# Optimization experiments

Hardware: AMD Instinct MI355X
Metric: run time of the kernel (lower is better)

## Reference

```python
import jax, jax.numpy as jnp
import numpy as np

NUM_USERS = 150000
NUM_ITEMS = 140000
NUM_BRANDS = 10000
N_NODES = NUM_USERS + NUM_ITEMS + NUM_BRANDS
EMBED_DIM = 64
N_LAYERS = 3
N_EDGES = 1200000


def setup_inputs() -> dict:
    key = jax.random.key(0)
    k1, k2, k3, k4, k5, k6 = jax.random.split(key, 6)
    # Xavier-uniform-ish init scale for embeddings
    s = float(np.sqrt(6.0 / (N_NODES + EMBED_DIM)))
    user_emb = jax.random.normal(k1, (NUM_USERS, EMBED_DIM), dtype=jnp.float32) * s
    item_emb = jax.random.normal(k2, (NUM_ITEMS, EMBED_DIM), dtype=jnp.float32) * s
    brand_emb = jax.random.normal(k3, (NUM_BRANDS, EMBED_DIM), dtype=jnp.float32) * s
    edge_src = jax.random.randint(k4, (N_EDGES,), 0, N_NODES, dtype=jnp.int32)
    edge_dst = jax.random.randint(k5, (N_EDGES,), 0, N_NODES, dtype=jnp.int32)
    # symmetric-normalized-adjacency-like positive values
    edge_vals = jax.random.uniform(k6, (N_EDGES,), dtype=jnp.float32)
    return {
        "user_emb": user_emb,
        "item_emb": item_emb,
        "brand_emb": brand_emb,
        "edge_vals": edge_vals,
        "edge_src": edge_src,
        "edge_dst": edge_dst,
    }


def _spmm(edge_src, edge_dst, edge_vals, x):
    # out[d] = sum_{e: dst[e]=d} vals[e] * x[src[e]]  (COO SpMM)
    msgs = x[edge_src] * edge_vals[:, None]  # [E, D]
    return jax.ops.segment_sum(msgs, edge_dst, num_segments=N_NODES)


def reference(user_emb, item_emb, brand_emb, edge_vals, edge_src, edge_dst):
    ego = jnp.concatenate([user_emb, item_emb, brand_emb], axis=0)  # [N, D]
    acc = ego
    h = ego
    for _ in range(N_LAYERS):
        h = _spmm(edge_src, edge_dst, edge_vals, h)
        acc = acc + h
    final = acc / jnp.float32(N_LAYERS + 1)  # mean over layer stack
    final_user = final[:NUM_USERS]
    final_item = final[NUM_USERS:NUM_USERS + NUM_ITEMS]
    return (final_user, final_item)
```

## Files before the change

kernel.cpp:

```cpp
#include <hip/hip_runtime.h>

#define NUM_USERS  150000
#define NUM_ITEMS  140000
#define NUM_BRANDS 10000
#define N_NODES    300000
#define DIM        64
#define N_EDGES    1200000
#define OUT_ROWS   290000

#define CHUNK      1024
#define NB         ((N_NODES + CHUNK - 1) / CHUNK)

#define NBIN       8
#define BINSZ      (N_EDGES / NBIN)

__device__ __forceinline__ float bf_lo(unsigned u) { return __uint_as_float(u << 16); }
__device__ __forceinline__ float bf_hi(unsigned u) { return __uint_as_float(u & 0xffff0000u); }
__device__ __forceinline__ unsigned pack_bf(float a, float b) {
    unsigned ua = __float_as_uint(a); ua += 0x7fffu + ((ua >> 16) & 1u);
    unsigned ub = __float_as_uint(b); ub += 0x7fffu + ((ub >> 16) & 1u);
    return (ua >> 16) | (ub & 0xffff0000u);
}

__global__ void lgcn_hist(const int* __restrict__ dst,
                          int* __restrict__ counts,
                          int* __restrict__ rank) {
    int e = blockIdx.x * blockDim.x + threadIdx.x;
    if (e >= N_EDGES) return;
    rank[e] = atomicAdd(&counts[dst[e]], 1);
}

__global__ void lgcn_scan_p1(const int* __restrict__ counts,
                             int* __restrict__ rowptr,
                             int* __restrict__ blockSums) {
    __shared__ int ts[256];
    int b    = blockIdx.x;
    int base = b * CHUNK;
    int t    = threadIdx.x;
    int c[4];
    int s = 0;
#pragma unroll
    for (int i = 0; i < 4; ++i) {
        int g = base + t * 4 + i;
        c[i] = (g < N_NODES) ? counts[g] : 0;
        s += c[i];
    }
    ts[t] = s;
    __syncthreads();
    for (int off = 1; off < 256; off <<= 1) {
        int v = (t >= off) ? ts[t - off] : 0;
        __syncthreads();
        ts[t] += v;
        __syncthreads();
    }
    int run = ts[t] - s;
#pragma unroll
    for (int i = 0; i < 4; ++i) {
        int g = base + t * 4 + i;
        if (g < N_NODES) rowptr[g] = run;
        run += c[i];
    }
    if (t == 255) blockSums[b] = ts[255];
}

__global__ void lgcn_scan_p2(int* __restrict__ blockSums) {
    __shared__ int sh[512];
    int t = threadIdx.x;
    int v = (t < NB) ? blockSums[t] : 0;
    sh[t] = v;
    __syncthreads();
    for (int off = 1; off < 512; off <<= 1) {
        int u = (t >= off) ? sh[t - off] : 0;
        __syncthreads();
        sh[t] += u;
        __syncthreads();
    }
    if (t < NB) blockSums[t] = sh[t] - v;
}

__global__ void lgcn_scan_p3(int* __restrict__ rowptr,
                             const int* __restrict__ blockSums) {
    int b    = blockIdx.x;
    int base = b * CHUNK;
    int t    = threadIdx.x;
    int off  = blockSums[b];
#pragma unroll
    for (int i = 0; i < 4; ++i) {
        int g = base + t * 4 + i;
        if (g < N_NODES) rowptr[g] += off;
    }
    if (b == 0 && t == 0) rowptr[N_NODES] = N_EDGES;
}

__global__ void lgcn_egobf(const float* __restrict__ user,
                           const float* __restrict__ item,
                           const float* __restrict__ brand,
                           uint4* __restrict__ ego_bf) {
    int g = blockIdx.x * blockDim.x + threadIdx.x;
    if (g >= N_NODES * 8) return;
    int row = g >> 3;
    int q   = g & 7;
    const float* srcp;
    if (row < NUM_USERS)                    srcp = user  + ((size_t)row << 6);
    else if (row < NUM_USERS + NUM_ITEMS)   srcp = item  + ((size_t)(row - NUM_USERS) << 6);
    else                                    srcp = brand + ((size_t)(row - NUM_USERS - NUM_ITEMS) << 6);
    float4 e0 = *(reinterpret_cast<const float4*>(srcp) + 2 * q);
    float4 e1 = *(reinterpret_cast<const float4*>(srcp) + 2 * q + 1);
    uint4 w;
    w.x = pack_bf(e0.x, e0.y);
    w.y = pack_bf(e0.z, e0.w);
    w.z = pack_bf(e1.x, e1.y);
    w.w = pack_bf(e1.z, e1.w);
    ego_bf[g] = w;
}

__global__ void lgcn_csr_bin(const int*   __restrict__ src,
                             const int*   __restrict__ dst,
                             const float* __restrict__ vals,
                             const int*   __restrict__ rank,
                             const int*   __restrict__ rowptr,
                             uint2*       __restrict__ csr) {
    int b    = blockIdx.x;
    int bin  = b & (NBIN - 1);
    int e    = (b >> 3) * blockDim.x + threadIdx.x;
    if (e >= N_EDGES) return;
    int pos = rowptr[dst[e]] + rank[e];
    int lo  = bin * BINSZ;
    if (pos >= lo && pos < lo + BINSZ) {
        csr[pos] = make_uint2((unsigned)src[e], __float_as_uint(vals[e]));
    }
}

__device__ __forceinline__ const float4* ego_row(const float* __restrict__ user,
                                                 const float* __restrict__ item,
                                                 const float* __restrict__ brand,
                                                 int r) {
    if (r < NUM_USERS)
        return reinterpret_cast<const float4*>(user) + (r << 4);
    else if (r < NUM_USERS + NUM_ITEMS)
        return reinterpret_cast<const float4*>(item) + ((r - NUM_USERS) << 4);
    else
        return reinterpret_cast<const float4*>(brand) + ((r - NUM_USERS - NUM_ITEMS) << 4);
}

template <int LAYER>
__global__ void lgcn_gather(const int*   __restrict__ rowptr,
                            const uint2* __restrict__ csr,
                            const uint4* __restrict__ h_src,
                            const float* __restrict__ user,
                            const float* __restrict__ item,
                            const float* __restrict__ brand,
                            const uint4* __restrict__ h1,
                            const uint4* __restrict__ h2,
                            uint4*       __restrict__ h_out,
                            float*       __restrict__ out) {
    int g    = blockIdx.x * blockDim.x + threadIdx.x;
    int node = g >> 3;
    int q    = g & 7;
    int beg = rowptr[node];
    int end = rowptr[node + 1];
    float4 s0 = make_float4(0.f, 0.f, 0.f, 0.f);
    float4 s1 = make_float4(0.f, 0.f, 0.f, 0.f);
    if (beg < end) {
        int last = end - 1;
        uint2 rec0 = csr[beg];
        uint2 rec1 = csr[beg + 1 < end ? beg + 1 : last];
        uint2 rec2 = csr[beg + 2 < end ? beg + 2 : last];
        uint2 rec3 = csr[beg + 3 < end ? beg + 3 : last];
        uint4 w0 = h_src[((int)rec0.x << 3) + q];
        uint4 w1 = h_src[((int)rec1.x << 3) + q];
        uint4 w2 = h_src[((int)rec2.x << 3) + q];
        for (int j = beg; j < end; ++j) {
            int jn = j + 4 < end ? j + 4 : last;
            uint2 rec4 = csr[jn];
            uint4 w3 = h_src[((int)rec3.x << 3) + q];
            float v = __uint_as_float(rec0.y);
            s0.x = fmaf(bf_lo(w0.x), v, s0.x);
            s0.y = fmaf(bf_hi(w0.x), v, s0.y);
            s0.z = fmaf(bf_lo(w0.y), v, s0.z);
            s0.w = fmaf(bf_hi(w0.y), v, s0.w);
            s1.x = fmaf(bf_lo(w0.z), v, s1.x);
            s1.y = fmaf(bf_hi(w0.z), v, s1.y);
            s1.z = fmaf(bf_lo(w0.w), v, s1.z);
            s1.w = fmaf(bf_hi(w0.w), v, s1.w);
            rec0 = rec1; rec1 = rec2; rec2 = rec3; rec3 = rec4;
            w0 = w1; w1 = w2; w2 = w3;
        }
    }
    if (LAYER != 3) {
        uint4 w;
        w.x = pack_bf(s0.x, s0.y);
        w.y = pack_bf(s0.z, s0.w);
        w.z = pack_bf(s1.x, s1.y);
        w.w = pack_bf(s1.z, s1.w);
        h_out[g] = w;
    } else if (node < OUT_ROWS) {
        const float4* er = ego_row(user, item, brand, node);
        float4 e0 = er[2 * q];
        float4 e1 = er[2 * q + 1];
        uint4 w1 = h1[g];
        uint4 w2 = h2[g];
        float4 o0, o1;
        o0.x = (e0.x + bf_lo(w1.x) + bf_lo(w2.x) + s0.x) * 0.25f;
        o0.y = (e0.y + bf_hi(w1.x) + bf_hi(w2.x) + s0.y) * 0.25f;
        o0.z = (e0.z + bf_lo(w1.y) + bf_lo(w2.y) + s0.z) * 0.25f;
        o0.w = (e0.w + bf_hi(w1.y) + bf_hi(w2.y) + s0.w) * 0.25f;
        o1.x = (e1.x + bf_lo(w1.z) + bf_lo(w2.z) + s1.x) * 0.25f;
        o1.y = (e1.y + bf_hi(w1.z) + bf_hi(w2.z) + s1.y) * 0.25f;
        o1.z = (e1.z + bf_lo(w1.w) + bf_lo(w2.w) + s1.z) * 0.25f;
        o1.w = (e1.w + bf_hi(w1.w) + bf_hi(w2.w) + s1.w) * 0.25f;
        float4* o = reinterpret_cast<float4*>(out) + g * 2;
        o[0] = o0;
        o[1] = o1;
    }
}

extern "C" void kernel_launch(void* const* d_in, const int* in_sizes, int n_in,
                              void* d_out, int out_size, void* d_ws, size_t ws_size,
                              hipStream_t stream) {
    const float* user  = (const float*)d_in[0];
    const float* item  = (const float*)d_in[1];
    const float* brand = (const float*)d_in[2];
    const float* vals  = (const float*)d_in[3];
    const int*   src   = (const int*)d_in[4];
    const int*   dst   = (const int*)d_in[5];
    float* out = (float*)d_out;

    size_t W = 0;
    uint4* ego_bf = (uint4*)d_ws;              W += (size_t)N_NODES * 32;
    uint4* h1  = (uint4*)((int*)d_ws + W);     W += (size_t)N_NODES * 32;
    uint4* h2  = (uint4*)((int*)d_ws + W);     W += (size_t)N_NODES * 32;
    uint2* csr = (uint2*)((int*)d_ws + W);     W += (size_t)N_EDGES * 2;
    int* rank      = (int*)d_ws + W;           W += N_EDGES;
    int* rowptr    = (int*)d_ws + W;           W += N_NODES + 2;
    int* counts    = (int*)d_ws + W;           W += N_NODES;
    int* blockSums = (int*)d_ws + W;           W += 512;
    (void)ws_size; (void)n_in; (void)in_sizes; (void)out_size;

    const int edgeBlocks   = (N_EDGES + 255) / 256;
    const int gatherBlocks = (N_NODES * 8) / 256;

    hipMemsetAsync(counts, 0, (size_t)N_NODES * sizeof(int), stream);

    lgcn_egobf  <<<gatherBlocks, 256, 0, stream>>>(user, item, brand, ego_bf);

    lgcn_hist   <<<edgeBlocks, 256, 0, stream>>>(dst, counts, rank);
    lgcn_scan_p1<<<NB, 256, 0, stream>>>(counts, rowptr, blockSums);
    lgcn_scan_p2<<<1, 512, 0, stream>>>(blockSums);
    lgcn_scan_p3<<<NB, 256, 0, stream>>>(rowptr, blockSums);
    lgcn_csr_bin<<<NBIN * edgeBlocks, 256, 0, stream>>>(src, dst, vals, rank,
                                                        rowptr, csr);

    lgcn_gather<1><<<gatherBlocks, 256, 0, stream>>>(rowptr, csr, ego_bf, user, item,
                                                     brand, h1, h2, h1, out);
    lgcn_gather<2><<<gatherBlocks, 256, 0, stream>>>(rowptr, csr, h1, user, item,
                                                     brand, h1, h2, h2, out);
    lgcn_gather<3><<<gatherBlocks, 256, 0, stream>>>(rowptr, csr, h2, user, item,
                                                     brand, h1, h2, nullptr, out);
}
```

Before: 273.7 us.

## Drop bf16 ego conversion, precompute CSR positions, unroll gather by two

```diff
diff --git a/kernel.cpp b/kernel.cpp
--- a/kernel.cpp
+++ b/kernel.cpp
@@ -92,42 +92,27 @@
     if (b == 0 && t == 0) rowptr[N_NODES] = N_EDGES;
 }
 
-__global__ void lgcn_egobf(const float* __restrict__ user,
-                           const float* __restrict__ item,
-                           const float* __restrict__ brand,
-                           uint4* __restrict__ ego_bf) {
-    int g = blockIdx.x * blockDim.x + threadIdx.x;
-    if (g >= N_NODES * 8) return;
-    int row = g >> 3;
-    int q   = g & 7;
-    const float* srcp;
-    if (row < NUM_USERS)                    srcp = user  + ((size_t)row << 6);
-    else if (row < NUM_USERS + NUM_ITEMS)   srcp = item  + ((size_t)(row - NUM_USERS) << 6);
-    else                                    srcp = brand + ((size_t)(row - NUM_USERS - NUM_ITEMS) << 6);
-    float4 e0 = *(reinterpret_cast<const float4*>(srcp) + 2 * q);
-    float4 e1 = *(reinterpret_cast<const float4*>(srcp) + 2 * q + 1);
-    uint4 w;
-    w.x = pack_bf(e0.x, e0.y);
-    w.y = pack_bf(e0.z, e0.w);
-    w.z = pack_bf(e1.x, e1.y);
-    w.w = pack_bf(e1.z, e1.w);
-    ego_bf[g] = w;
+__global__ void lgcn_pos(const int* __restrict__ dst,
+                         const int* __restrict__ rank,
+                         const int* __restrict__ rowptr,
+                         int* __restrict__ pos) {
+    int e = blockIdx.x * blockDim.x + threadIdx.x;
+    if (e >= N_EDGES) return;
+    pos[e] = rowptr[dst[e]] + rank[e];
 }
 
 __global__ void lgcn_csr_bin(const int*   __restrict__ src,
-                             const int*   __restrict__ dst,
                              const float* __restrict__ vals,
-                             const int*   __restrict__ rank,
-                             const int*   __restrict__ rowptr,
+                             const int*   __restrict__ pos,
                              uint2*       __restrict__ csr) {
     int b    = blockIdx.x;
     int bin  = b & (NBIN - 1);
     int e    = (b >> 3) * blockDim.x + threadIdx.x;
     if (e >= N_EDGES) return;
-    int pos = rowptr[dst[e]] + rank[e];
-    int lo  = bin * BINSZ;
-    if (pos >= lo && pos < lo + BINSZ) {
-        csr[pos] = make_uint2((unsigned)src[e], __float_as_uint(vals[e]));
+    int p  = pos[e];
+    int lo = bin * BINSZ;
+    if (p >= lo && p < lo + BINSZ) {
+        csr[p] = make_uint2((unsigned)src[e], __float_as_uint(vals[e]));
     }
 }
 
@@ -142,6 +127,53 @@
     else
         return reinterpret_cast<const float4*>(brand) + ((r - NUM_USERS - NUM_ITEMS) << 4);
 }
+
+template <int LAYER>
+struct RowStore {
+    typedef uint4 type;
+    static __device__ __forceinline__ type load(const uint4* __restrict__ h,
+                                                const float*, const float*, const float*,
+                                                int r, int q) {
+        return h[(r << 3) + q];
+    }
+    static __device__ __forceinline__ void fma(float4& s0, float4& s1, type w, float v) {
+        s0.x = fmaf(bf_lo(w.x), v, s0.x);
+        s0.y = fmaf(bf_hi(w.x), v, s0.y);
+        s0.z = fmaf(bf_lo(w.y), v, s0.z);
+        s0.w = fmaf(bf_hi(w.y), v, s0.w);
+        s1.x = fmaf(bf_lo(w.z), v, s1.x);
+        s1.y = fmaf(bf_hi(w.z), v, s1.y);
+        s1.z = fmaf(bf_lo(w.w), v, s1.z);
+        s1.w = fmaf(bf_hi(w.w), v, s1.w);
+    }
+};
+
+struct Row8 { float4 a, b; };
+template <>
+struct RowStore<1> {
+    typedef Row8 type;
+    static __device__ __forceinline__ type load(const uint4*,
+                                                const float* __restrict__ u,
+                                                const float* __restrict__ i,
+                                                const float* __restrict__ b,
+                                                int r, int q) {
+        const float4* er = ego_row(u, i, b, r);
+        Row8 t;
+        t.a = er[2 * q];
+        t.b = er[2 * q + 1];
+        return t;
+    }
+    static __device__ __forceinline__ void fma(float4& s0, float4& s1, type w, float v) {
+        s0.x = fmaf(w.a.x, v, s0.x);
+        s0.y = fmaf(w.a.y, v, s0.y);
+        s0.z = fmaf(w.a.z, v, s0.z);
+        s0.w = fmaf(w.a.w, v, s0.w);
+        s1.x = fmaf(w.b.x, v, s1.x);
+        s1.y = fmaf(w.b.y, v, s1.y);
+        s1.z = fmaf(w.b.z, v, s1.z);
+        s1.w = fmaf(w.b.w, v, s1.w);
+    }
+};
 
 template <int LAYER>
 __global__ void lgcn_gather(const int*   __restrict__ rowptr,
@@ -154,6 +186,7 @@
                             const uint4* __restrict__ h2,
                             uint4*       __restrict__ h_out,
                             float*       __restrict__ out) {
+    typedef typename RowStore<LAYER>::type RowT;
     int g    = blockIdx.x * blockDim.x + threadIdx.x;
     int node = g >> 3;
     int q    = g & 7;
@@ -161,31 +194,30 @@
     int end = rowptr[node + 1];
     float4 s0 = make_float4(0.f, 0.f, 0.f, 0.f);
     float4 s1 = make_float4(0.f, 0.f, 0.f, 0.f);
+    float4 t0 = make_float4(0.f, 0.f, 0.f, 0.f);
+    float4 t1 = make_float4(0.f, 0.f, 0.f, 0.f);
     if (beg < end) {
         int last = end - 1;
-        uint2 rec0 = csr[beg];
-        uint2 rec1 = csr[beg + 1 < end ? beg + 1 : last];
-        uint2 rec2 = csr[beg + 2 < end ? beg + 2 : last];
-        uint2 rec3 = csr[beg + 3 < end ? beg + 3 : last];
-        uint4 w0 = h_src[((int)rec0.x << 3) + q];
-        uint4 w1 = h_src[((int)rec1.x << 3) + q];
-        uint4 w2 = h_src[((int)rec2.x << 3) + q];
-        for (int j = beg; j < end; ++j) {
-            int jn = j + 4 < end ? j + 4 : last;
-            uint2 rec4 = csr[jn];
-            uint4 w3 = h_src[((int)rec3.x << 3) + q];
-            float v = __uint_as_float(rec0.y);
-            s0.x = fmaf(bf_lo(w0.x), v, s0.x);
-            s0.y = fmaf(bf_hi(w0.x), v, s0.y);
-            s0.z = fmaf(bf_lo(w0.y), v, s0.z);
-            s0.w = fmaf(bf_hi(w0.y), v, s0.w);
-            s1.x = fmaf(bf_lo(w0.z), v, s1.x);
-            s1.y = fmaf(bf_hi(w0.z), v, s1.y);
-            s1.z = fmaf(bf_lo(w0.w), v, s1.z);
-            s1.w = fmaf(bf_hi(w0.w), v, s1.w);
-            rec0 = rec1; rec1 = rec2; rec2 = rec3; rec3 = rec4;
-            w0 = w1; w1 = w2; w2 = w3;
+        uint2 r0 = csr[beg];
+        uint2 r1 = csr[beg + 1 < end ? beg + 1 : last];
+        uint2 r2 = csr[beg + 2 < end ? beg + 2 : last];
+        uint2 r3 = csr[beg + 3 < end ? beg + 3 : last];
+        RowT wA = RowStore<LAYER>::load(h_src, user, item, brand, (int)r0.x, q);
+        RowT wB = RowStore<LAYER>::load(h_src, user, item, brand, (int)r1.x, q);
+        for (int j = beg; j < end; j += 2) {
+            uint2 r4 = csr[j + 4 < end ? j + 4 : last];
+            uint2 r5 = csr[j + 5 < end ? j + 5 : last];
+            RowT wC = RowStore<LAYER>::load(h_src, user, item, brand, (int)r2.x, q);
+            RowT wD = RowStore<LAYER>::load(h_src, user, item, brand, (int)r3.x, q);
+            float vA = __uint_as_float(r0.y);
+            float vB = (j + 1 < end) ? __uint_as_float(r1.y) : 0.f;
+            RowStore<LAYER>::fma(s0, s1, wA, vA);
+            RowStore<LAYER>::fma(t0, t1, wB, vB);
+            r0 = r2; r1 = r3; r2 = r4; r3 = r5;
+            wA = wC; wB = wD;
         }
+        s0.x += t0.x; s0.y += t0.y; s0.z += t0.z; s0.w += t0.w;
+        s1.x += t1.x; s1.y += t1.y; s1.z += t1.z; s1.w += t1.w;
     }
     if (LAYER != 3) {
         uint4 w;
@@ -227,11 +259,11 @@
     float* out = (float*)d_out;
 
     size_t W = 0;
-    uint4* ego_bf = (uint4*)d_ws;              W += (size_t)N_NODES * 32;
-    uint4* h1  = (uint4*)((int*)d_ws + W);     W += (size_t)N_NODES * 32;
+    uint4* h1  = (uint4*)d_ws;                 W += (size_t)N_NODES * 32;
     uint4* h2  = (uint4*)((int*)d_ws + W);     W += (size_t)N_NODES * 32;
     uint2* csr = (uint2*)((int*)d_ws + W);     W += (size_t)N_EDGES * 2;
     int* rank      = (int*)d_ws + W;           W += N_EDGES;
+    int* pos       = (int*)d_ws + W;           W += N_EDGES;
     int* rowptr    = (int*)d_ws + W;           W += N_NODES + 2;
     int* counts    = (int*)d_ws + W;           W += N_NODES;
     int* blockSums = (int*)d_ws + W;           W += 512;
@@ -242,16 +274,14 @@
 
     hipMemsetAsync(counts, 0, (size_t)N_NODES * sizeof(int), stream);
 
-    lgcn_egobf  <<<gatherBlocks, 256, 0, stream>>>(user, item, brand, ego_bf);
-
     lgcn_hist   <<<edgeBlocks, 256, 0, stream>>>(dst, counts, rank);
     lgcn_scan_p1<<<NB, 256, 0, stream>>>(counts, rowptr, blockSums);
     lgcn_scan_p2<<<1, 512, 0, stream>>>(blockSums);
     lgcn_scan_p3<<<NB, 256, 0, stream>>>(rowptr, blockSums);
-    lgcn_csr_bin<<<NBIN * edgeBlocks, 256, 0, stream>>>(src, dst, vals, rank,
-                                                        rowptr, csr);
-
-    lgcn_gather<1><<<gatherBlocks, 256, 0, stream>>>(rowptr, csr, ego_bf, user, item,
+    lgcn_pos    <<<edgeBlocks, 256, 0, stream>>>(dst, rank, rowptr, pos);
+    lgcn_csr_bin<<<NBIN * edgeBlocks, 256, 0, stream>>>(src, vals, pos, csr);
+
+    lgcn_gather<1><<<gatherBlocks, 256, 0, stream>>>(rowptr, csr, nullptr, user, item,
                                                      brand, h1, h2, h1, out);
     lgcn_gather<2><<<gatherBlocks, 256, 0, stream>>>(rowptr, csr, h1, user, item,
                                                      brand, h1, h2, h2, out);
```

Measured after the change: 241.0 us. -12.0%, faster.

## Drop bf16 ego conversion, gather fp32 ego directly, precompute CSR positions

Applied to the files above, without the earlier changes.

```diff
diff --git a/kernel.cpp b/kernel.cpp
--- a/kernel.cpp
+++ b/kernel.cpp
@@ -92,42 +92,27 @@
     if (b == 0 && t == 0) rowptr[N_NODES] = N_EDGES;
 }
 
-__global__ void lgcn_egobf(const float* __restrict__ user,
-                           const float* __restrict__ item,
-                           const float* __restrict__ brand,
-                           uint4* __restrict__ ego_bf) {
-    int g = blockIdx.x * blockDim.x + threadIdx.x;
-    if (g >= N_NODES * 8) return;
-    int row = g >> 3;
-    int q   = g & 7;
-    const float* srcp;
-    if (row < NUM_USERS)                    srcp = user  + ((size_t)row << 6);
-    else if (row < NUM_USERS + NUM_ITEMS)   srcp = item  + ((size_t)(row - NUM_USERS) << 6);
-    else                                    srcp = brand + ((size_t)(row - NUM_USERS - NUM_ITEMS) << 6);
-    float4 e0 = *(reinterpret_cast<const float4*>(srcp) + 2 * q);
-    float4 e1 = *(reinterpret_cast<const float4*>(srcp) + 2 * q + 1);
-    uint4 w;
-    w.x = pack_bf(e0.x, e0.y);
-    w.y = pack_bf(e0.z, e0.w);
-    w.z = pack_bf(e1.x, e1.y);
-    w.w = pack_bf(e1.z, e1.w);
-    ego_bf[g] = w;
+__global__ void lgcn_pos(const int* __restrict__ dst,
+                         const int* __restrict__ rank,
+                         const int* __restrict__ rowptr,
+                         int* __restrict__ pos) {
+    int e = blockIdx.x * blockDim.x + threadIdx.x;
+    if (e >= N_EDGES) return;
+    pos[e] = rowptr[dst[e]] + rank[e];
 }
 
 __global__ void lgcn_csr_bin(const int*   __restrict__ src,
-                             const int*   __restrict__ dst,
                              const float* __restrict__ vals,
-                             const int*   __restrict__ rank,
-                             const int*   __restrict__ rowptr,
+                             const int*   __restrict__ pos,
                              uint2*       __restrict__ csr) {
     int b    = blockIdx.x;
     int bin  = b & (NBIN - 1);
     int e    = (b >> 3) * blockDim.x + threadIdx.x;
     if (e >= N_EDGES) return;
-    int pos = rowptr[dst[e]] + rank[e];
-    int lo  = bin * BINSZ;
-    if (pos >= lo && pos < lo + BINSZ) {
-        csr[pos] = make_uint2((unsigned)src[e], __float_as_uint(vals[e]));
+    int p  = pos[e];
+    int lo = bin * BINSZ;
+    if (p >= lo && p < lo + BINSZ) {
+        csr[p] = make_uint2((unsigned)src[e], __float_as_uint(vals[e]));
     }
 }
 
@@ -143,17 +128,13 @@
         return reinterpret_cast<const float4*>(brand) + ((r - NUM_USERS - NUM_ITEMS) << 4);
 }
 
-template <int LAYER>
-__global__ void lgcn_gather(const int*   __restrict__ rowptr,
-                            const uint2* __restrict__ csr,
-                            const uint4* __restrict__ h_src,
-                            const float* __restrict__ user,
-                            const float* __restrict__ item,
-                            const float* __restrict__ brand,
-                            const uint4* __restrict__ h1,
-                            const uint4* __restrict__ h2,
-                            uint4*       __restrict__ h_out,
-                            float*       __restrict__ out) {
+__global__ void __launch_bounds__(256, 8)
+lgcn_gather1(const int*   __restrict__ rowptr,
+             const uint2* __restrict__ csr,
+             const float* __restrict__ user,
+             const float* __restrict__ item,
+             const float* __restrict__ brand,
+             uint4*       __restrict__ h_out) {
     int g    = blockIdx.x * blockDim.x + threadIdx.x;
     int node = g >> 3;
     int q    = g & 7;
@@ -162,44 +143,111 @@
     float4 s0 = make_float4(0.f, 0.f, 0.f, 0.f);
     float4 s1 = make_float4(0.f, 0.f, 0.f, 0.f);
     if (beg < end) {
-        int last = end - 1;
         uint2 rec0 = csr[beg];
-        uint2 rec1 = csr[beg + 1 < end ? beg + 1 : last];
-        uint2 rec2 = csr[beg + 2 < end ? beg + 2 : last];
-        uint2 rec3 = csr[beg + 3 < end ? beg + 3 : last];
-        uint4 w0 = h_src[((int)rec0.x << 3) + q];
-        uint4 w1 = h_src[((int)rec1.x << 3) + q];
-        uint4 w2 = h_src[((int)rec2.x << 3) + q];
+        uint2 rec1 = csr[(beg + 1 < end) ? beg + 1 : beg];
+        const float4* p0 = ego_row(user, item, brand, (int)rec0.x);
+        float4 a0 = p0[2 * q];
+        float4 b0 = p0[2 * q + 1];
         for (int j = beg; j < end; ++j) {
-            int jn = j + 4 < end ? j + 4 : last;
-            uint2 rec4 = csr[jn];
-            uint4 w3 = h_src[((int)rec3.x << 3) + q];
+            int jn = j + 2 < end ? j + 2 : end - 1;
+            uint2 rec2 = csr[jn];
+            const float4* p1 = ego_row(user, item, brand, (int)rec1.x);
+            float4 a1 = p1[2 * q];
+            float4 b1 = p1[2 * q + 1];
             float v = __uint_as_float(rec0.y);
-            s0.x = fmaf(bf_lo(w0.x), v, s0.x);
-            s0.y = fmaf(bf_hi(w0.x), v, s0.y);
-            s0.z = fmaf(bf_lo(w0.y), v, s0.z);
-            s0.w = fmaf(bf_hi(w0.y), v, s0.w);
-            s1.x = fmaf(bf_lo(w0.z), v, s1.x);
-            s1.y = fmaf(bf_hi(w0.z), v, s1.y);
-            s1.z = fmaf(bf_lo(w0.w), v, s1.z);
-            s1.w = fmaf(bf_hi(w0.w), v, s1.w);
-            rec0 = rec1; rec1 = rec2; rec2 = rec3; rec3 = rec4;
-            w0 = w1; w1 = w2; w2 = w3;
+            s0.x = fmaf(a0.x, v, s0.x);
+            s0.y = fmaf(a0.y, v, s0.y);
+            s0.z = fmaf(a0.z, v, s0.z);
+            s0.w = fmaf(a0.w, v, s0.w);
+            s1.x = fmaf(b0.x, v, s1.x);
+            s1.y = fmaf(b0.y, v, s1.y);
+            s1.z = fmaf(b0.z, v, s1.z);
+            s1.w = fmaf(b0.w, v, s1.w);
+            rec0 = rec1; rec1 = rec2; a0 = a1; b0 = b1;
         }
     }
-    if (LAYER != 3) {
-        uint4 w;
-        w.x = pack_bf(s0.x, s0.y);
-        w.y = pack_bf(s0.z, s0.w);
-        w.z = pack_bf(s1.x, s1.y);
-        w.w = pack_bf(s1.z, s1.w);
-        h_out[g] = w;
-    } else if (node < OUT_ROWS) {
+    uint4 w;
+    w.x = pack_bf(s0.x, s0.y);
+    w.y = pack_bf(s0.z, s0.w);
+    w.z = pack_bf(s1.x, s1.y);
+    w.w = pack_bf(s1.z, s1.w);
+    h_out[g] = w;
+}
+
+__device__ __forceinline__ void gather_bf_core(int beg, int end, int q,
+                                               const uint2* __restrict__ csr,
+                                               const uint4* __restrict__ h_src,
+                                               float4& s0, float4& s1) {
+    int last = end - 1;
+    uint2 rec0 = csr[beg];
+    uint2 rec1 = csr[beg + 1 < end ? beg + 1 : last];
+    uint2 rec2 = csr[beg + 2 < end ? beg + 2 : last];
+    uint2 rec3 = csr[beg + 3 < end ? beg + 3 : last];
+    uint4 w0 = h_src[((int)rec0.x << 3) + q];
+    uint4 w1 = h_src[((int)rec1.x << 3) + q];
+    uint4 w2 = h_src[((int)rec2.x << 3) + q];
+    for (int j = beg; j < end; ++j) {
+        int jn = j + 4 < end ? j + 4 : last;
+        uint2 rec4 = csr[jn];
+        uint4 w3 = h_src[((int)rec3.x << 3) + q];
+        float v = __uint_as_float(rec0.y);
+        s0.x = fmaf(bf_lo(w0.x), v, s0.x);
+        s0.y = fmaf(bf_hi(w0.x), v, s0.y);
+        s0.z = fmaf(bf_lo(w0.y), v, s0.z);
+        s0.w = fmaf(bf_hi(w0.y), v, s0.w);
+        s1.x = fmaf(bf_lo(w0.z), v, s1.x);
+        s1.y = fmaf(bf_hi(w0.z), v, s1.y);
+        s1.z = fmaf(bf_lo(w0.w), v, s1.z);
+        s1.w = fmaf(bf_hi(w0.w), v, s1.w);
+        rec0 = rec1; rec1 = rec2; rec2 = rec3; rec3 = rec4;
+        w0 = w1; w1 = w2; w2 = w3;
+    }
+}
+
+__global__ void __launch_bounds__(256, 8)
+lgcn_gather2(const int*   __restrict__ rowptr,
+             const uint2* __restrict__ csr,
+             const uint4* __restrict__ h_src,
+             uint4*       __restrict__ h_out) {
+    int g    = blockIdx.x * blockDim.x + threadIdx.x;
+    int node = g >> 3;
+    int q    = g & 7;
+    int beg = rowptr[node];
+    int end = rowptr[node + 1];
+    float4 s0 = make_float4(0.f, 0.f, 0.f, 0.f);
+    float4 s1 = make_float4(0.f, 0.f, 0.f, 0.f);
+    if (beg < end) gather_bf_core(beg, end, q, csr, h_src, s0, s1);
+    uint4 w;
+    w.x = pack_bf(s0.x, s0.y);
+    w.y = pack_bf(s0.z, s0.w);
+    w.z = pack_bf(s1.x, s1.y);
+    w.w = pack_bf(s1.z, s1.w);
+    h_out[g] = w;
+}
+
+__global__ void __launch_bounds__(256, 8)
+lgcn_gather3(const int*   __restrict__ rowptr,
+             const uint2* __restrict__ csr,
+             const uint4* __restrict__ h_src,
+             const float* __restrict__ user,
+             const float* __restrict__ item,
+             const float* __restrict__ brand,
+             const uint4* __restrict__ h1,
+             float*       __restrict__ out) {
+    int g    = blockIdx.x * blockDim.x + threadIdx.x;
+    int node = g >> 3;
+    int q    = g & 7;
+    int beg = rowptr[node];
+    int end = rowptr[node + 1];
+    float4 s0 = make_float4(0.f, 0.f, 0.f, 0.f);
+    float4 s1 = make_float4(0.f, 0.f, 0.f, 0.f);
+    if (beg < end) gather_bf_core(beg, end, q, csr, h_src, s0, s1);
+    if (node < OUT_ROWS) {
         const float4* er = ego_row(user, item, brand, node);
         float4 e0 = er[2 * q];
         float4 e1 = er[2 * q + 1];
         uint4 w1 = h1[g];
-        uint4 w2 = h2[g];
+        uint4 w2 = h_src[g];
         float4 o0, o1;
         o0.x = (e0.x + bf_lo(w1.x) + bf_lo(w2.x) + s0.x) * 0.25f;
         o0.y = (e0.y + bf_hi(w1.x) + bf_hi(w2.x) + s0.y) * 0.25f;
@@ -227,11 +275,11 @@
     float* out = (float*)d_out;
 
     size_t W = 0;
-    uint4* ego_bf = (uint4*)d_ws;              W += (size_t)N_NODES * 32;
-    uint4* h1  = (uint4*)((int*)d_ws + W);     W += (size_t)N_NODES * 32;
+    uint4* h1  = (uint4*)d_ws;                 W += (size_t)N_NODES * 32;
     uint4* h2  = (uint4*)((int*)d_ws + W);     W += (size_t)N_NODES * 32;
     uint2* csr = (uint2*)((int*)d_ws + W);     W += (size_t)N_EDGES * 2;
     int* rank      = (int*)d_ws + W;           W += N_EDGES;
+    int* pos       = (int*)d_ws + W;           W += N_EDGES;
     int* rowptr    = (int*)d_ws + W;           W += N_NODES + 2;
     int* counts    = (int*)d_ws + W;           W += N_NODES;
     int* blockSums = (int*)d_ws + W;           W += 512;
@@ -242,19 +290,15 @@
 
     hipMemsetAsync(counts, 0, (size_t)N_NODES * sizeof(int), stream);
 
-    lgcn_egobf  <<<gatherBlocks, 256, 0, stream>>>(user, item, brand, ego_bf);
-
     lgcn_hist   <<<edgeBlocks, 256, 0, stream>>>(dst, counts, rank);
     lgcn_scan_p1<<<NB, 256, 0, stream>>>(counts, rowptr, blockSums);
     lgcn_scan_p2<<<1, 512, 0, stream>>>(blockSums);
     lgcn_scan_p3<<<NB, 256, 0, stream>>>(rowptr, blockSums);
-    lgcn_csr_bin<<<NBIN * edgeBlocks, 256, 0, stream>>>(src, dst, vals, rank,
-                                                        rowptr, csr);
-
-    lgcn_gather<1><<<gatherBlocks, 256, 0, stream>>>(rowptr, csr, ego_bf, user, item,
-                                                     brand, h1, h2, h1, out);
-    lgcn_gather<2><<<gatherBlocks, 256, 0, stream>>>(rowptr, csr, h1, user, item,
-                                                     brand, h1, h2, h2, out);
-    lgcn_gather<3><<<gatherBlocks, 256, 0, stream>>>(rowptr, csr, h2, user, item,
-                                                     brand, h1, h2, nullptr, out);
-}
+    lgcn_pos    <<<edgeBlocks, 256, 0, stream>>>(dst, rank, rowptr, pos);
+    lgcn_csr_bin<<<NBIN * edgeBlocks, 256, 0, stream>>>(src, vals, pos, csr);
+
+    lgcn_gather1<<<gatherBlocks, 256, 0, stream>>>(rowptr, csr, user, item, brand, h1);
+    lgcn_gather2<<<gatherBlocks, 256, 0, stream>>>(rowptr, csr, h1, h2);
+    lgcn_gather3<<<gatherBlocks, 256, 0, stream>>>(rowptr, csr, h2, user, item, brand,
+                                                   h1, out);
+}
```

After: 246.1 us. 10.1% less time.
